# Kernel optimization log

Hardware: AMD Instinct MI355X
Metric: run time of the kernel (lower is better)

The kernel has to match this reference:

```python
import jax, jax.numpy as jnp
import numpy as np

NUM_HEADS = 12
HEAD_SIZE = 64
HIDDEN = NUM_HEADS * HEAD_SIZE  # 768
ONE_SIDED_WINDOW = 256          # attention_window 512 // 2
NEG = -10000.0


def setup_inputs() -> dict:
    key = jax.random.key(0)
    ks = jax.random.split(key, 16)
    B, W, E, H = 1, 2048, 128, HIDDEN
    std = 0.02
    def lin(kw, kb):
        return (jax.random.normal(kw, (H, H), jnp.float32) * std,
                jax.random.normal(kb, (H,), jnp.float32) * std)
    q_w, q_b = lin(ks[0], ks[1])
    k_w, k_b = lin(ks[2], ks[3])
    v_w, v_b = lin(ks[4], ks[5])
    w2e_w, w2e_b = lin(ks[6], ks[7])
    e2w_w, e2w_b = lin(ks[8], ks[9])
    e2e_w, e2e_b = lin(ks[10], ks[11])
    return {
        "word_hidden_states": jax.random.normal(ks[12], (B, W, H), jnp.float32),
        "entity_hidden_states": jax.random.normal(ks[13], (B, E, H), jnp.float32),
        "attention_mask": jnp.zeros((B, 1, 1, W + E), jnp.float32),
        "q_w": q_w, "q_b": q_b, "k_w": k_w, "k_b": k_b, "v_w": v_w, "v_b": v_b,
        "w2e_w": w2e_w, "w2e_b": w2e_b, "e2w_w": e2w_w, "e2w_b": e2w_b,
        "e2e_w": e2e_w, "e2e_b": e2e_b,
    }


def reference(word_hidden_states, entity_hidden_states, attention_mask,
              q_w, q_b, k_w, k_b, v_w, v_b,
              w2e_w, w2e_b, e2w_w, e2w_b, e2e_w, e2e_b):
    B, W, H = word_hidden_states.shape
    E = entity_hidden_states.shape[1]
    S = W + E

    def heads(x):  # [B, L, H] -> [B, nh, L, hd]
        return x.reshape(B, -1, NUM_HEADS, HEAD_SIZE).transpose(0, 2, 1, 3)

    concat = jnp.concatenate([word_hidden_states, entity_hidden_states], axis=1)
    k = heads(concat @ k_w + k_b)          # [B, nh, S, hd]
    v = heads(concat @ v_w + v_b)
    q_w2w = heads(word_hidden_states @ q_w + q_b)
    q_w2e = heads(word_hidden_states @ w2e_w + w2e_b)
    q_e2w = heads(entity_hidden_states @ e2w_w + e2w_b)
    q_e2e = heads(entity_hidden_states @ e2e_w + e2e_b)

    k_word, k_ent = k[:, :, :W], k[:, :, W:]

    # --- w2w: Longformer sliding-window QK^T, then _conversion to a dense
    # [B, nh, W, W] matrix with out-of-band entries set to -10000. ---
    w2w = jnp.einsum('bhid,bhjd->bhij', q_w2w, k_word)  # [B, nh, W, W]
    idx = jnp.arange(W)
    in_band = jnp.abs(idx[:, None] - idx[None, :]) <= ONE_SIDED_WINDOW  # [W, W]
    # diagonal mask: float_mask[j] (-10000 where attention_mask != 0) added
    # within the band (broadcast over heads / query positions)
    mask_words = attention_mask[:, 0, 0, :W]                # [B, W]
    float_mask = jnp.where(mask_words != 0.0, NEG, 0.0)     # [B, W]
    w2w = w2w + float_mask[:, None, None, :]
    # _conversion: out-of-band -> -10000; also exact zeros -> -10000 (source quirk)
    w2w = jnp.where(in_band[None, None] & (w2w != 0.0), w2w, NEG)

    # --- entity-aware dense blocks ---
    w2e = jnp.einsum('bhid,bhjd->bhij', q_w2e, k_ent)    # [B, nh, W, E]
    e2w = jnp.einsum('bhid,bhjd->bhij', q_e2w, k_word)   # [B, nh, E, W]
    e2e = jnp.einsum('bhid,bhjd->bhij', q_e2e, k_ent)    # [B, nh, E, E]

    word_scores = jnp.concatenate([w2w, w2e], axis=3)    # [B, nh, W, S]
    ent_scores = jnp.concatenate([e2w, e2e], axis=3)     # [B, nh, E, S]
    scores = jnp.concatenate([word_scores, ent_scores], axis=2)  # [B, nh, S, S]

    scores = scores / jnp.sqrt(jnp.float32(HEAD_SIZE)) + attention_mask
    probs = jax.nn.softmax(scores, axis=-1)

    ctx = jnp.einsum('bhij,bhjd->bhid', probs, v)        # [B, nh, S, hd]
    ctx = ctx.transpose(0, 2, 1, 3).reshape(B, S, H)
    return ctx[:, :W, :], ctx[:, W:, :]
```

## Files before the change

kernel.cpp:

```cpp
#include <hip/hip_runtime.h>

typedef __bf16 bf16x8 __attribute__((ext_vector_type(8)));
typedef unsigned short u16x8 __attribute__((ext_vector_type(8)));
typedef u16x8 u16x8_a __attribute__((may_alias));
typedef unsigned int u32x2 __attribute__((ext_vector_type(2)));
typedef u32x2 u32x2_a __attribute__((may_alias));
typedef unsigned int u32x4 __attribute__((ext_vector_type(4)));
typedef u32x4 u32x4_a __attribute__((may_alias));
typedef float f32x4 __attribute__((ext_vector_type(4)));

#define LOG2E 1.4426950408889634f
#define NEGV  -10000.0f

__device__ __forceinline__ unsigned short f2bf(float f){
  union{float f; unsigned int i;} x; x.f=f;
  unsigned int i = x.i;
  return (unsigned short)((i + 0x7FFFu + ((i>>16)&1u)) >> 16);
}
__device__ __forceinline__ u16x8 cvt8(float4 a, float4 b){
  u16x8 r;
  r[0]=f2bf(a.x); r[1]=f2bf(a.y); r[2]=f2bf(a.z); r[3]=f2bf(a.w);
  r[4]=f2bf(b.x); r[5]=f2bf(b.y); r[6]=f2bf(b.z); r[7]=f2bf(b.w);
  return r;
}
__device__ __forceinline__ bf16x8 ldb(const unsigned short* p){
  return __builtin_bit_cast(bf16x8, *(const u16x8_a*)p);
}

__global__ __launch_bounds__(256) void cast_a(
    const float* __restrict__ word, const float* __restrict__ ent,
    unsigned short* __restrict__ Abf)
{
  size_t e = ((size_t)blockIdx.x*256 + threadIdx.x)*8;
  const size_t WE = (size_t)2048*768;
  const float* s = (e < WE) ? (word + e) : (ent + (e - WE));
  float4 a = *(const float4*)s;
  float4 b = *(const float4*)(s+4);
  *(u16x8_a*)(Abf + e) = cvt8(a,b);
}

__global__ __launch_bounds__(256) void transpose6(
    const float* __restrict__ w0, const float* __restrict__ w1,
    const float* __restrict__ w2, const float* __restrict__ w3,
    const float* __restrict__ w4, const float* __restrict__ w5,
    unsigned short* __restrict__ outT)
{
  const float* src;
  switch (blockIdx.z){
    case 0: src = w0; break; case 1: src = w1; break; case 2: src = w2; break;
    case 3: src = w3; break; case 4: src = w4; break; default: src = w5; break;
  }
  unsigned short* dst = outT + (size_t)blockIdx.z * 589824;
  __shared__ float tile[32][33];
  int tx = threadIdx.x, ty = threadIdx.y;
  int x0 = blockIdx.x*32, y0 = blockIdx.y*32;
  #pragma unroll
  for (int i=0;i<32;i+=8) tile[ty+i][tx] = src[(size_t)(y0+ty+i)*768 + x0+tx];
  __syncthreads();
  #pragma unroll
  for (int i=0;i<32;i+=8) dst[(size_t)(x0+ty+i)*768 + y0+tx] = f2bf(tile[tx][ty+i]);
}

__global__ __launch_bounds__(256) void transpose_v(
    const unsigned short* __restrict__ Vb, unsigned short* __restrict__ VbT)
{
  __shared__ unsigned short t[32][33];
  int tx = threadIdx.x, ty = threadIdx.y;
  int x0 = blockIdx.x*32;
  int y0 = blockIdx.y*32;
  #pragma unroll
  for (int i=0;i<32;i+=8) t[ty+i][tx] = Vb[(size_t)(x0+ty+i)*768 + y0+tx];
  __syncthreads();
  #pragma unroll
  for (int i=0;i<32;i+=8) VbT[(size_t)(y0+ty+i)*2176 + x0+tx] = t[tx][ty+i];
}

__global__ __launch_bounds__(256) void gemm_proj(
    const unsigned short* __restrict__ Abf,
    const unsigned short* __restrict__ wT,
    const float* __restrict__ bK, const float* __restrict__ bV,
    const float* __restrict__ bQ, const float* __restrict__ bWE,
    const float* __restrict__ bEW, const float* __restrict__ bEE,
    unsigned short* __restrict__ oK, unsigned short* __restrict__ oV,
    unsigned short* __restrict__ oQ, unsigned short* __restrict__ oWE,
    unsigned short* __restrict__ oEW, unsigned short* __restrict__ oEE)
{
  int mt = blockIdx.x, ntile = blockIdx.y;
  int g, mg;
  if      (mt <  34){ g=0; mg=mt;     }
  else if (mt <  68){ g=1; mg=mt-34;  }
  else if (mt < 100){ g=2; mg=mt-68;  }
  else if (mt < 132){ g=3; mg=mt-100; }
  else if (mt < 134){ g=4; mg=mt-132; }
  else              { g=5; mg=mt-134; }
  int m0 = mg*64;
  const unsigned short* A = Abf + (size_t)((g>=4 ? 2048 : 0) + m0)*768;
  const unsigned short* B = wT + (size_t)g*589824;
  const float* bias; unsigned short* out;
  switch (g){
    case 0: bias=bK;  out=oK;  break;
    case 1: bias=bV;  out=oV;  break;
    case 2: bias=bQ;  out=oQ;  break;
    case 3: bias=bWE; out=oWE; break;
    case 4: bias=bEW; out=oEW; break;
    default:bias=bEE; out=oEE; break;
  }
  out += (size_t)m0*768;
  int n0 = ntile*128;

  __shared__ __align__(16) unsigned short a_s[64*32];
  __shared__ __align__(16) unsigned short b_s[128*32];

  int tid  = threadIdx.x;
  int w    = tid>>6, lane = tid&63, quad = lane>>4, lr = lane&15;
  int wm   = (w&1)*32, wn = (w>>1)*64;

  f32x4 acc[2][4];
  #pragma unroll
  for (int i=0;i<2;i++) for (int j=0;j<4;j++) for (int r=0;r<4;r++) acc[i][j][r]=0.f;

  int ar  = tid>>1;
  int ak2 = (tid&1)*16;
  int aar = tid>>2;
  int aak = (tid&3)*8;
  const unsigned short* Arow = A + (size_t)aar*768 + aak;
  const unsigned short* Brow = B + (size_t)(n0+ar)*768 + ak2;

  for (int k0=0; k0<768; k0+=32){
    u16x8 av  = *(const u16x8_a*)(Arow + k0);
    u16x8 bv0 = *(const u16x8_a*)(Brow + k0);
    u16x8 bv1 = *(const u16x8_a*)(Brow + k0 + 8);
    __syncthreads();
    *(u16x8_a*)(a_s + aar*32 + aak)    = av;
    *(u16x8_a*)(b_s + ar*32 + ak2)     = bv0;
    *(u16x8_a*)(b_s + ar*32 + ak2 + 8) = bv1;
    __syncthreads();
    bf16x8 af[2], bfr[4];
    #pragma unroll
    for (int i=0;i<2;i++) af[i]  = ldb(a_s + (wm+i*16+lr)*32 + quad*8);
    #pragma unroll
    for (int j=0;j<4;j++) bfr[j] = ldb(b_s + (wn+j*16+lr)*32 + quad*8);
    #pragma unroll
    for (int i=0;i<2;i++)
      #pragma unroll
      for (int j=0;j<4;j++)
        acc[i][j] = __builtin_amdgcn_mfma_f32_16x16x32_bf16(af[i], bfr[j], acc[i][j], 0,0,0);
  }
  #pragma unroll
  for (int j=0;j<4;j++){
    int col = n0 + wn + j*16 + lr;
    float bb = bias[col];
    #pragma unroll
    for (int i=0;i<2;i++){
      int rowb = wm + i*16 + quad*4;
      #pragma unroll
      for (int r=0;r<4;r++)
        out[(size_t)(rowb+r)*768 + col] = f2bf(acc[i][j][r] + bb);
    }
  }
}

__global__ __launch_bounds__(256) void attn_split(
  const unsigned short* __restrict__ Kb,  const unsigned short* __restrict__ VbT,
  const unsigned short* __restrict__ Qw,  const unsigned short* __restrict__ Qwe,
  const unsigned short* __restrict__ Qew, const unsigned short* __restrict__ Qee,
  const float* __restrict__ am,
  float* __restrict__ outw, float* __restrict__ pO, float* __restrict__ pML)
{
  int lin = blockIdx.x + 80*blockIdx.y;
  int wid = (lin & 7)*120 + (lin >> 3);
  int bx = wid % 80;
  int h  = wid / 80;

  int tid = threadIdx.x, w = tid>>6, lane = tid&63, quad = lane>>4, lr = lane&15;
  bool isword = bx < 64;
  int qrb, kh, nsplit, eg=0, ehalf=0;
  const unsigned short *Qa, *Qb;
  if (isword){ qrb = bx*32 + (w>>1)*16; kh = w&1; nsplit = 2; Qa=Qw;  Qb=Qwe; }
  else       { int e = bx-64; eg = e>>1; ehalf = e&1;
               qrb = eg*16;             kh = w;   nsplit = 4; Qa=Qew; Qb=Qee; }
  int hofs = h*64;

  __shared__ __align__(16) unsigned int shb[4*64*20];
  unsigned int* p32w = shb + w*320;

  const unsigned short* qr = Qa + (size_t)(qrb+lr)*768 + hofs + quad*8;
  bf16x8 qa0 = ldb(qr), qa1 = ldb(qr + 32);
  qr = Qb + (size_t)(qrb+lr)*768 + hofs + quad*8;
  bf16x8 qb0 = ldb(qr), qb1 = ldb(qr + 32);

  u16x8 onesu;
  #pragma unroll
  for (int i=0;i<8;i++) onesu[i] = 0x3F80;
  bf16x8 onesf = __builtin_bit_cast(bf16x8, onesu);

  float m = -1e30f;
  f32x4 o[4], l4;
  #pragma unroll
  for (int r=0;r<4;r++) l4[r] = 0.f;
  #pragma unroll
  for (int n2=0;n2<4;n2++) for (int r=0;r<4;r++) o[n2][r] = 0.f;

  int lo, nw, start, end, step;
  if (isword){
    lo = qrb - 256; if (lo < 0) lo = 0; lo &= ~31;
    int hi = qrb + 272; if (hi > 2048) hi = 2048; hi = (hi + 31) & ~31;
    nw = (hi - lo) >> 5;
    start = kh; end = nw + 4; step = 2;
  } else {
    lo = 0; nw = 64;
    start = ehalf*34 + kh; end = ehalf*34 + 34; step = 4;
  }
  int iq = qrb + lr;

  for (int c = start; c < end; c += step){
    bool entp = c >= nw;
    int j0 = entp ? (2048 + (c-nw)*32) : (lo + c*32);

    const unsigned short* kp = Kb + (size_t)(j0+lr)*768 + hofs + quad*8;
    bf16x8 k00 = ldb(kp),          k01 = ldb(kp + 32);
    bf16x8 k10 = ldb(kp + 16*768), k11 = ldb(kp + 16*768 + 32);
    const unsigned short* vp = VbT + (size_t)(hofs + lr)*2176 + j0 + quad*8;
    bf16x8 va0 = ldb(vp), va1 = ldb(vp + 16*2176), va2 = ldb(vp + 32*2176), va3 = ldb(vp + 48*2176);
    float4 am0 = *(const float4*)(am + j0 + quad*4);
    float4 am1 = *(const float4*)(am + j0 + 16 + quad*4);

    bf16x8 qf0 = entp ? qb0 : qa0;
    bf16x8 qf1 = entp ? qb1 : qa1;
    f32x4 st0 = {0.f,0.f,0.f,0.f}, st1 = {0.f,0.f,0.f,0.f};
    __builtin_amdgcn_s_setprio(1);
    st0 = __builtin_amdgcn_mfma_f32_16x16x32_bf16(k00, qf0, st0, 0,0,0);
    st0 = __builtin_amdgcn_mfma_f32_16x16x32_bf16(k01, qf1, st0, 0,0,0);
    st1 = __builtin_amdgcn_mfma_f32_16x16x32_bf16(k10, qf0, st1, 0,0,0);
    st1 = __builtin_amdgcn_mfma_f32_16x16x32_bf16(k11, qf1, st1, 0,0,0);
    __builtin_amdgcn_s_setprio(0);

    float sc0[4], sc1[4];
    bool wband = isword && !entp;
    #pragma unroll
    for (int r=0;r<4;r++){
      {
        float amj = am0[r];
        float sv  = st0[r];
        if (wband){
          sv += (amj != 0.f) ? NEGV : 0.f;
          int j = j0 + quad*4 + r;
          bool ok = ((unsigned)(iq - j + 256) <= 512u) && (sv != 0.f);
          sv = ok ? sv : NEGV;
        }
        sc0[r] = sv * (LOG2E*0.125f) + amj * LOG2E;
      }
      {
        float amj = am1[r];
        float sv  = st1[r];
        if (wband){
          sv += (amj != 0.f) ? NEGV : 0.f;
          int j = j0 + 16 + quad*4 + r;
          bool ok = ((unsigned)(iq - j + 256) <= 512u) && (sv != 0.f);
          sv = ok ? sv : NEGV;
        }
        sc1[r] = sv * (LOG2E*0.125f) + amj * LOG2E;
      }
    }

    float mx = fmaxf(fmaxf(fmaxf(sc0[0],sc0[1]), fmaxf(sc0[2],sc0[3])),
                     fmaxf(fmaxf(sc1[0],sc1[1]), fmaxf(sc1[2],sc1[3])));
    mx = fmaxf(mx, __shfl_xor(mx, 16));
    mx = fmaxf(mx, __shfl_xor(mx, 32));
    float mn = fmaxf(m, mx);
    float alpha = exp2f(m - mn);
    m = mn;

    float p00 = exp2f(sc0[0]-mn), p01 = exp2f(sc0[1]-mn);
    float p02 = exp2f(sc0[2]-mn), p03 = exp2f(sc0[3]-mn);
    float p10 = exp2f(sc1[0]-mn), p11 = exp2f(sc1[1]-mn);
    float p12 = exp2f(sc1[2]-mn), p13 = exp2f(sc1[3]-mn);
    unsigned int x0 = (unsigned int)f2bf(p00) | ((unsigned int)f2bf(p01)<<16);
    unsigned int x1 = (unsigned int)f2bf(p02) | ((unsigned int)f2bf(p03)<<16);
    unsigned int x2 = (unsigned int)f2bf(p10) | ((unsigned int)f2bf(p11)<<16);
    unsigned int x3 = (unsigned int)f2bf(p12) | ((unsigned int)f2bf(p13)<<16);

    #pragma unroll
    for (int r=0;r<4;r++) l4[r] *= alpha;
    #pragma unroll
    for (int n2=0;n2<4;n2++)
      #pragma unroll
      for (int r=0;r<4;r++) o[n2][r] *= alpha;

    unsigned int* row = p32w + lr*20;
    u32x2 w0v = {x0, x1};
    u32x2 w1v = {x2, x3};
    *(u32x2_a*)(row + quad*2)     = w0v;
    *(u32x2_a*)(row + 8 + quad*2) = w1v;
    bf16x8 pf = ldb((const unsigned short*)(p32w + lr*20 + quad*4));

    __builtin_amdgcn_s_setprio(1);
    o[0] = __builtin_amdgcn_mfma_f32_16x16x32_bf16(va0, pf, o[0], 0,0,0);
    o[1] = __builtin_amdgcn_mfma_f32_16x16x32_bf16(va1, pf, o[1], 0,0,0);
    o[2] = __builtin_amdgcn_mfma_f32_16x16x32_bf16(va2, pf, o[2], 0,0,0);
    o[3] = __builtin_amdgcn_mfma_f32_16x16x32_bf16(va3, pf, o[3], 0,0,0);
    l4   = __builtin_amdgcn_mfma_f32_16x16x32_bf16(onesf, pf, l4, 0,0,0);
    __builtin_amdgcn_s_setprio(0);
  }

  float lsc = l4[0];
  __syncthreads();
  {
    float* my = (float*)shb + ((size_t)(w*64 + lane))*20;
    my[0] = m; my[1] = lsc;
    #pragma unroll
    for (int n2=0;n2<4;n2++)
      #pragma unroll
      for (int r=0;r<4;r++) my[2+n2*4+r] = o[n2][r];
  }
  __syncthreads();
  if (kh == 0){
    for (int p=1; p<nsplit; p++){
      const float* pr = (float*)shb + ((size_t)((w+p)*64 + lane))*20;
      float m2 = pr[0], l2 = pr[1];
      float M  = fmaxf(m, m2);
      float e1 = exp2f(m-M), e2 = exp2f(m2-M);
      m = M;
      lsc = lsc*e1 + l2*e2;
      #pragma unroll
      for (int n2=0;n2<4;n2++)
        #pragma unroll
        for (int r=0;r<4;r++)
          o[n2][r] = o[n2][r]*e1 + pr[2+n2*4+r]*e2;
    }
    if (isword){
      float rinv = 1.f / lsc;
      #pragma unroll
      for (int n2=0;n2<4;n2++){
        float4 sv;
        sv.x = o[n2][0]*rinv; sv.y = o[n2][1]*rinv;
        sv.z = o[n2][2]*rinv; sv.w = o[n2][3]*rinv;
        *(float4*)(outw + (size_t)(qrb+lr)*768 + hofs + n2*16 + quad*4) = sv;
      }
    } else {
      int idx = (eg*12 + h)*2 + ehalf;
      float* po = pO + (size_t)idx*1024;
      #pragma unroll
      for (int n2=0;n2<4;n2++){
        float4 sv;
        sv.x = o[n2][0]; sv.y = o[n2][1]; sv.z = o[n2][2]; sv.w = o[n2][3];
        *(float4*)(po + lr*64 + n2*16 + quad*4) = sv;
      }
      if (quad == 0){
        float* pml = pML + (size_t)idx*32;
        pml[lr*2]     = m;
        pml[lr*2 + 1] = lsc;
      }
    }
  }
}

__global__ __launch_bounds__(256) void merge_ent(
    const float* __restrict__ pO, const float* __restrict__ pML,
    float* __restrict__ oute)
{
  int b = blockIdx.x;
  int g = b/12, h = b%12;
  int tid = threadIdx.x;
  int row = tid>>4, cg = tid&15;
  int i0 = b*2, i1 = b*2+1;
  float m0 = pML[(size_t)i0*32 + row*2], l0 = pML[(size_t)i0*32 + row*2 + 1];
  float m1 = pML[(size_t)i1*32 + row*2], l1 = pML[(size_t)i1*32 + row*2 + 1];
  float M  = fmaxf(m0, m1);
  float e0 = exp2f(m0-M), e1 = exp2f(m1-M);
  float rl = 1.f/(l0*e0 + l1*e1);
  float4 a = *(const float4*)(pO + (size_t)i0*1024 + row*64 + cg*4);
  float4 c = *(const float4*)(pO + (size_t)i1*1024 + row*64 + cg*4);
  float4 o;
  o.x = (a.x*e0 + c.x*e1)*rl;
  o.y = (a.y*e0 + c.y*e1)*rl;
  o.z = (a.z*e0 + c.z*e1)*rl;
  o.w = (a.w*e0 + c.w*e1)*rl;
  *(float4*)(oute + (size_t)(g*16+row)*768 + h*64 + cg*4) = o;
}

extern "C" void kernel_launch(void* const* d_in, const int* in_sizes, int n_in,
                              void* d_out, int out_size, void* d_ws, size_t ws_size,
                              hipStream_t stream) {
  const float* word  = (const float*)d_in[0];
  const float* ent   = (const float*)d_in[1];
  const float* am    = (const float*)d_in[2];
  const float* q_w   = (const float*)d_in[3];
  const float* q_b   = (const float*)d_in[4];
  const float* k_w   = (const float*)d_in[5];
  const float* k_b   = (const float*)d_in[6];
  const float* v_w   = (const float*)d_in[7];
  const float* v_b   = (const float*)d_in[8];
  const float* w2e_w = (const float*)d_in[9];
  const float* w2e_b = (const float*)d_in[10];
  const float* e2w_w = (const float*)d_in[11];
  const float* e2w_b = (const float*)d_in[12];
  const float* e2e_w = (const float*)d_in[13];
  const float* e2e_b = (const float*)d_in[14];

  unsigned short* ws  = (unsigned short*)d_ws;
  unsigned short* wT  = ws;
  unsigned short* Kb  = wT  + (size_t)6*589824;
  unsigned short* Vb  = Kb  + (size_t)2176*768;
  unsigned short* Qw  = Vb  + (size_t)2176*768;
  unsigned short* Qwe = Qw  + (size_t)2048*768;
  unsigned short* Qew = Qwe + (size_t)2048*768;
  unsigned short* Qee = Qew + (size_t)128*768;
  unsigned short* VbT = Qee + (size_t)128*768;
  unsigned short* Abf = VbT + (size_t)768*2176;

  float* pO  = (float*)wT;
  float* pML = pO + (size_t)192*1024;

  float* outw = (float*)d_out;
  float* oute = outw + (size_t)2048*768;

  hipLaunchKernelGGL(cast_a, dim3(816), dim3(256), 0, stream, word, ent, Abf);
  hipLaunchKernelGGL(transpose6, dim3(24,24,6), dim3(32,8), 0, stream,
                     k_w, v_w, q_w, w2e_w, e2w_w, e2e_w, wT);
  hipLaunchKernelGGL(gemm_proj, dim3(136,6), dim3(256), 0, stream,
                     Abf, wT, k_b, v_b, q_b, w2e_b, e2w_b, e2e_b,
                     Kb, Vb, Qw, Qwe, Qew, Qee);
  hipLaunchKernelGGL(transpose_v, dim3(68,24), dim3(32,8), 0, stream, Vb, VbT);
  hipLaunchKernelGGL(attn_split, dim3(80,12), dim3(256), 0, stream,
                     Kb, VbT, Qw, Qwe, Qew, Qee, am, outw, pO, pML);
  hipLaunchKernelGGL(merge_ent, dim3(96), dim3(256), 0, stream,
                     pO, pML, oute);
}
```

Before: 180.6 us.

## Process two key chunks per attention iteration and use direct global-to-LDS loads in GEMM

The attention loop now handles two 32-key chunks per iteration. It issues both sets of K loads up front, computes one shared running max and rescale, and does two PV MFMA passes, with the second V load issued between them. This halves the per-chunk softmax rescale and reduction overhead and adds memory-level parallelism, at the cost of more registers and a masked tail when the chunk count is odd. The projection GEMM replaces its register-staged global-to-LDS copies with global_load_lds direct transfers, and the LDS stride for the partial-result merge is padded to 21.

```diff
diff --git a/kernel.cpp b/kernel.cpp
--- a/kernel.cpp
+++ b/kernel.cpp
@@ -25,6 +25,11 @@
 }
 __device__ __forceinline__ bf16x8 ldb(const unsigned short* p){
   return __builtin_bit_cast(bf16x8, *(const u16x8_a*)p);
+}
+__device__ __forceinline__ void gload16(const unsigned short* g, unsigned short* l){
+  __builtin_amdgcn_global_load_lds(
+    (const __attribute__((address_space(1))) void*)g,
+    (__attribute__((address_space(3))) void*)l, 16, 0, 0);
 }
 
 __global__ __launch_bounds__(256) void cast_a(
@@ -119,21 +124,20 @@
   #pragma unroll
   for (int i=0;i<2;i++) for (int j=0;j<4;j++) for (int r=0;r<4;r++) acc[i][j][r]=0.f;
 
-  int ar  = tid>>1;
-  int ak2 = (tid&1)*16;
-  int aar = tid>>2;
-  int aak = (tid&3)*8;
-  const unsigned short* Arow = A + (size_t)aar*768 + aak;
-  const unsigned short* Brow = B + (size_t)(n0+ar)*768 + ak2;
+  int srow = lane>>2;
+  int scol = (lane&3)*8;
+  const unsigned short* gA  = A + (size_t)(w*16 + srow)*768 + scol;
+  const unsigned short* gB0 = B + (size_t)(n0 + w*32 + srow)*768 + scol;
+  const unsigned short* gB1 = gB0 + (size_t)16*768;
+  unsigned short* lA  = a_s + w*16*32;
+  unsigned short* lB0 = b_s + w*32*32;
+  unsigned short* lB1 = b_s + w*32*32 + 16*32;
 
   for (int k0=0; k0<768; k0+=32){
-    u16x8 av  = *(const u16x8_a*)(Arow + k0);
-    u16x8 bv0 = *(const u16x8_a*)(Brow + k0);
-    u16x8 bv1 = *(const u16x8_a*)(Brow + k0 + 8);
     __syncthreads();
-    *(u16x8_a*)(a_s + aar*32 + aak)    = av;
-    *(u16x8_a*)(b_s + ar*32 + ak2)     = bv0;
-    *(u16x8_a*)(b_s + ar*32 + ak2 + 8) = bv1;
+    gload16(gA  + k0, lA);
+    gload16(gB0 + k0, lB0);
+    gload16(gB1 + k0, lB1);
     __syncthreads();
     bf16x8 af[2], bfr[4];
     #pragma unroll
@@ -181,8 +185,8 @@
                qrb = eg*16;             kh = w;   nsplit = 4; Qa=Qew; Qb=Qee; }
   int hofs = h*64;
 
-  __shared__ __align__(16) unsigned int shb[4*64*20];
-  unsigned int* p32w = shb + w*320;
+  __shared__ __align__(16) unsigned int shb[4*64*21];
+  unsigned int* p32w = shb + w*(16*44);
 
   const unsigned short* qr = Qa + (size_t)(qrb+lr)*768 + hofs + quad*8;
   bf16x8 qa0 = ldb(qr), qa1 = ldb(qr + 32);
@@ -213,72 +217,97 @@
   }
   int iq = qrb + lr;
 
-  for (int c = start; c < end; c += step){
-    bool entp = c >= nw;
-    int j0 = entp ? (2048 + (c-nw)*32) : (lo + c*32);
-
-    const unsigned short* kp = Kb + (size_t)(j0+lr)*768 + hofs + quad*8;
-    bf16x8 k00 = ldb(kp),          k01 = ldb(kp + 32);
-    bf16x8 k10 = ldb(kp + 16*768), k11 = ldb(kp + 16*768 + 32);
-    const unsigned short* vp = VbT + (size_t)(hofs + lr)*2176 + j0 + quad*8;
-    bf16x8 va0 = ldb(vp), va1 = ldb(vp + 16*2176), va2 = ldb(vp + 32*2176), va3 = ldb(vp + 48*2176);
-    float4 am0 = *(const float4*)(am + j0 + quad*4);
-    float4 am1 = *(const float4*)(am + j0 + 16 + quad*4);
-
-    bf16x8 qf0 = entp ? qb0 : qa0;
-    bf16x8 qf1 = entp ? qb1 : qa1;
-    f32x4 st0 = {0.f,0.f,0.f,0.f}, st1 = {0.f,0.f,0.f,0.f};
+  for (int c = start; c < end; c += 2*step){
+    int c2r = c + step;
+    bool ph = (c2r >= end);
+    int c2 = ph ? c : c2r;
+
+    bool entp1 = c  >= nw;  int j1 = entp1 ? (2048 + (c -nw)*32) : (lo + c *32);
+    bool entp2 = c2 >= nw;  int j2 = entp2 ? (2048 + (c2-nw)*32) : (lo + c2*32);
+
+    const unsigned short* kp1 = Kb + (size_t)(j1+lr)*768 + hofs + quad*8;
+    bf16x8 kA0 = ldb(kp1),          kA1 = ldb(kp1 + 32);
+    bf16x8 kA2 = ldb(kp1 + 16*768), kA3 = ldb(kp1 + 16*768 + 32);
+    const unsigned short* kp2 = Kb + (size_t)(j2+lr)*768 + hofs + quad*8;
+    bf16x8 kB0 = ldb(kp2),          kB1 = ldb(kp2 + 32);
+    bf16x8 kB2 = ldb(kp2 + 16*768), kB3 = ldb(kp2 + 16*768 + 32);
+    const unsigned short* vp1 = VbT + (size_t)(hofs + lr)*2176 + j1 + quad*8;
+    bf16x8 v10 = ldb(vp1), v11 = ldb(vp1 + 16*2176), v12 = ldb(vp1 + 32*2176), v13 = ldb(vp1 + 48*2176);
+    float4 amA0 = *(const float4*)(am + j1 + quad*4);
+    float4 amA1 = *(const float4*)(am + j1 + 16 + quad*4);
+    float4 amB0 = *(const float4*)(am + j2 + quad*4);
+    float4 amB1 = *(const float4*)(am + j2 + 16 + quad*4);
+
+    bf16x8 qf10 = entp1 ? qb0 : qa0, qf11 = entp1 ? qb1 : qa1;
+    bf16x8 qf20 = entp2 ? qb0 : qa0, qf21 = entp2 ? qb1 : qa1;
+
+    f32x4 sA0 = {0.f,0.f,0.f,0.f}, sA1 = {0.f,0.f,0.f,0.f};
+    f32x4 sB0 = {0.f,0.f,0.f,0.f}, sB1 = {0.f,0.f,0.f,0.f};
     __builtin_amdgcn_s_setprio(1);
-    st0 = __builtin_amdgcn_mfma_f32_16x16x32_bf16(k00, qf0, st0, 0,0,0);
-    st0 = __builtin_amdgcn_mfma_f32_16x16x32_bf16(k01, qf1, st0, 0,0,0);
-    st1 = __builtin_amdgcn_mfma_f32_16x16x32_bf16(k10, qf0, st1, 0,0,0);
-    st1 = __builtin_amdgcn_mfma_f32_16x16x32_bf16(k11, qf1, st1, 0,0,0);
+    sA0 = __builtin_amdgcn_mfma_f32_16x16x32_bf16(kA0, qf10, sA0, 0,0,0);
+    sA0 = __builtin_amdgcn_mfma_f32_16x16x32_bf16(kA1, qf11, sA0, 0,0,0);
+    sA1 = __builtin_amdgcn_mfma_f32_16x16x32_bf16(kA2, qf10, sA1, 0,0,0);
+    sA1 = __builtin_amdgcn_mfma_f32_16x16x32_bf16(kA3, qf11, sA1, 0,0,0);
+    sB0 = __builtin_amdgcn_mfma_f32_16x16x32_bf16(kB0, qf20, sB0, 0,0,0);
+    sB0 = __builtin_amdgcn_mfma_f32_16x16x32_bf16(kB1, qf21, sB0, 0,0,0);
+    sB1 = __builtin_amdgcn_mfma_f32_16x16x32_bf16(kB2, qf20, sB1, 0,0,0);
+    sB1 = __builtin_amdgcn_mfma_f32_16x16x32_bf16(kB3, qf21, sB1, 0,0,0);
     __builtin_amdgcn_s_setprio(0);
 
-    float sc0[4], sc1[4];
-    bool wband = isword && !entp;
+    float scA0[4], scA1[4], scB0[4], scB1[4];
+    bool wb1 = isword && !entp1;
+    bool wb2 = isword && !entp2;
     #pragma unroll
     for (int r=0;r<4;r++){
-      {
-        float amj = am0[r];
-        float sv  = st0[r];
-        if (wband){
-          sv += (amj != 0.f) ? NEGV : 0.f;
-          int j = j0 + quad*4 + r;
+      { float amj = amA0[r], sv = sA0[r];
+        if (wb1){ sv += (amj != 0.f) ? NEGV : 0.f;
+          int j = j1 + quad*4 + r;
           bool ok = ((unsigned)(iq - j + 256) <= 512u) && (sv != 0.f);
-          sv = ok ? sv : NEGV;
-        }
-        sc0[r] = sv * (LOG2E*0.125f) + amj * LOG2E;
-      }
-      {
-        float amj = am1[r];
-        float sv  = st1[r];
-        if (wband){
-          sv += (amj != 0.f) ? NEGV : 0.f;
-          int j = j0 + 16 + quad*4 + r;
+          sv = ok ? sv : NEGV; }
+        scA0[r] = sv * (LOG2E*0.125f) + amj * LOG2E; }
+      { float amj = amA1[r], sv = sA1[r];
+        if (wb1){ sv += (amj != 0.f) ? NEGV : 0.f;
+          int j = j1 + 16 + quad*4 + r;
           bool ok = ((unsigned)(iq - j + 256) <= 512u) && (sv != 0.f);
-          sv = ok ? sv : NEGV;
-        }
-        sc1[r] = sv * (LOG2E*0.125f) + amj * LOG2E;
-      }
+          sv = ok ? sv : NEGV; }
+        scA1[r] = sv * (LOG2E*0.125f) + amj * LOG2E; }
+      { float amj = amB0[r], sv = sB0[r];
+        if (wb2){ sv += (amj != 0.f) ? NEGV : 0.f;
+          int j = j2 + quad*4 + r;
+          bool ok = ((unsigned)(iq - j + 256) <= 512u) && (sv != 0.f);
+          sv = ok ? sv : NEGV; }
+        scB0[r] = sv * (LOG2E*0.125f) + amj * LOG2E; }
+      { float amj = amB1[r], sv = sB1[r];
+        if (wb2){ sv += (amj != 0.f) ? NEGV : 0.f;
+          int j = j2 + 16 + quad*4 + r;
+          bool ok = ((unsigned)(iq - j + 256) <= 512u) && (sv != 0.f);
+          sv = ok ? sv : NEGV; }
+        scB1[r] = sv * (LOG2E*0.125f) + amj * LOG2E; }
     }
-
-    float mx = fmaxf(fmaxf(fmaxf(sc0[0],sc0[1]), fmaxf(sc0[2],sc0[3])),
-                     fmaxf(fmaxf(sc1[0],sc1[1]), fmaxf(sc1[2],sc1[3])));
+    if (ph){
+      #pragma unroll
+      for (int r=0;r<4;r++){ scB0[r] = -1e30f; scB1[r] = -1e30f; }
+    }
+
+    float mx = fmaxf(
+      fmaxf(fmaxf(fmaxf(scA0[0],scA0[1]), fmaxf(scA0[2],scA0[3])),
+            fmaxf(fmaxf(scA1[0],scA1[1]), fmaxf(scA1[2],scA1[3]))),
+      fmaxf(fmaxf(fmaxf(scB0[0],scB0[1]), fmaxf(scB0[2],scB0[3])),
+            fmaxf(fmaxf(scB1[0],scB1[1]), fmaxf(scB1[2],scB1[3]))));
     mx = fmaxf(mx, __shfl_xor(mx, 16));
     mx = fmaxf(mx, __shfl_xor(mx, 32));
     float mn = fmaxf(m, mx);
     float alpha = exp2f(m - mn);
     m = mn;
 
-    float p00 = exp2f(sc0[0]-mn), p01 = exp2f(sc0[1]-mn);
-    float p02 = exp2f(sc0[2]-mn), p03 = exp2f(sc0[3]-mn);
-    float p10 = exp2f(sc1[0]-mn), p11 = exp2f(sc1[1]-mn);
-    float p12 = exp2f(sc1[2]-mn), p13 = exp2f(sc1[3]-mn);
-    unsigned int x0 = (unsigned int)f2bf(p00) | ((unsigned int)f2bf(p01)<<16);
-    unsigned int x1 = (unsigned int)f2bf(p02) | ((unsigned int)f2bf(p03)<<16);
-    unsigned int x2 = (unsigned int)f2bf(p10) | ((unsigned int)f2bf(p11)<<16);
-    unsigned int x3 = (unsigned int)f2bf(p12) | ((unsigned int)f2bf(p13)<<16);
+    unsigned int xA0 = (unsigned int)f2bf(exp2f(scA0[0]-mn)) | ((unsigned int)f2bf(exp2f(scA0[1]-mn))<<16);
+    unsigned int xA1 = (unsigned int)f2bf(exp2f(scA0[2]-mn)) | ((unsigned int)f2bf(exp2f(scA0[3]-mn))<<16);
+    unsigned int xA2 = (unsigned int)f2bf(exp2f(scA1[0]-mn)) | ((unsigned int)f2bf(exp2f(scA1[1]-mn))<<16);
+    unsigned int xA3 = (unsigned int)f2bf(exp2f(scA1[2]-mn)) | ((unsigned int)f2bf(exp2f(scA1[3]-mn))<<16);
+    unsigned int xB0 = (unsigned int)f2bf(exp2f(scB0[0]-mn)) | ((unsigned int)f2bf(exp2f(scB0[1]-mn))<<16);
+    unsigned int xB1 = (unsigned int)f2bf(exp2f(scB0[2]-mn)) | ((unsigned int)f2bf(exp2f(scB0[3]-mn))<<16);
+    unsigned int xB2 = (unsigned int)f2bf(exp2f(scB1[0]-mn)) | ((unsigned int)f2bf(exp2f(scB1[1]-mn))<<16);
+    unsigned int xB3 = (unsigned int)f2bf(exp2f(scB1[2]-mn)) | ((unsigned int)f2bf(exp2f(scB1[3]-mn))<<16);
 
     #pragma unroll
     for (int r=0;r<4;r++) l4[r] *= alpha;
@@ -287,26 +316,42 @@
       #pragma unroll
       for (int r=0;r<4;r++) o[n2][r] *= alpha;
 
-    unsigned int* row = p32w + lr*20;
-    u32x2 w0v = {x0, x1};
-    u32x2 w1v = {x2, x3};
-    *(u32x2_a*)(row + quad*2)     = w0v;
-    *(u32x2_a*)(row + 8 + quad*2) = w1v;
-    bf16x8 pf = ldb((const unsigned short*)(p32w + lr*20 + quad*4));
+    unsigned int* row = p32w + lr*44;
+    u32x2 wv0 = {xA0, xA1};
+    u32x2 wv1 = {xA2, xA3};
+    u32x2 wv2 = {xB0, xB1};
+    u32x2 wv3 = {xB2, xB3};
+    *(u32x2_a*)(row + quad*2)      = wv0;
+    *(u32x2_a*)(row + 8  + quad*2) = wv1;
+    *(u32x2_a*)(row + 16 + quad*2) = wv2;
+    *(u32x2_a*)(row + 24 + quad*2) = wv3;
+    bf16x8 pf1 = ldb((const unsigned short*)(p32w + lr*44 + quad*4));
+    bf16x8 pf2 = ldb((const unsigned short*)(p32w + lr*44 + 16 + quad*4));
 
     __builtin_amdgcn_s_setprio(1);
-    o[0] = __builtin_amdgcn_mfma_f32_16x16x32_bf16(va0, pf, o[0], 0,0,0);
-    o[1] = __builtin_amdgcn_mfma_f32_16x16x32_bf16(va1, pf, o[1], 0,0,0);
-    o[2] = __builtin_amdgcn_mfma_f32_16x16x32_bf16(va2, pf, o[2], 0,0,0);
-    o[3] = __builtin_amdgcn_mfma_f32_16x16x32_bf16(va3, pf, o[3], 0,0,0);
-    l4   = __builtin_amdgcn_mfma_f32_16x16x32_bf16(onesf, pf, l4, 0,0,0);
+    o[0] = __builtin_amdgcn_mfma_f32_16x16x32_bf16(v10, pf1, o[0], 0,0,0);
+    o[1] = __builtin_amdgcn_mfma_f32_16x16x32_bf16(v11, pf1, o[1], 0,0,0);
+    o[2] = __builtin_amdgcn_mfma_f32_16x16x32_bf16(v12, pf1, o[2], 0,0,0);
+    o[3] = __builtin_amdgcn_mfma_f32_16x16x32_bf16(v13, pf1, o[3], 0,0,0);
+    l4   = __builtin_amdgcn_mfma_f32_16x16x32_bf16(onesf, pf1, l4, 0,0,0);
+    __builtin_amdgcn_s_setprio(0);
+
+    const unsigned short* vp2 = VbT + (size_t)(hofs + lr)*2176 + j2 + quad*8;
+    bf16x8 v20 = ldb(vp2), v21 = ldb(vp2 + 16*2176), v22 = ldb(vp2 + 32*2176), v23 = ldb(vp2 + 48*2176);
+
+    __builtin_amdgcn_s_setprio(1);
+    o[0] = __builtin_amdgcn_mfma_f32_16x16x32_bf16(v20, pf2, o[0], 0,0,0);
+    o[1] = __builtin_amdgcn_mfma_f32_16x16x32_bf16(v21, pf2, o[1], 0,0,0);
+    o[2] = __builtin_amdgcn_mfma_f32_16x16x32_bf16(v22, pf2, o[2], 0,0,0);
+    o[3] = __builtin_amdgcn_mfma_f32_16x16x32_bf16(v23, pf2, o[3], 0,0,0);
+    l4   = __builtin_amdgcn_mfma_f32_16x16x32_bf16(onesf, pf2, l4, 0,0,0);
     __builtin_amdgcn_s_setprio(0);
   }
 
   float lsc = l4[0];
   __syncthreads();
   {
-    float* my = (float*)shb + ((size_t)(w*64 + lane))*20;
+    float* my = (float*)shb + ((size_t)(w*64 + lane))*21;
     my[0] = m; my[1] = lsc;
     #pragma unroll
     for (int n2=0;n2<4;n2++)
@@ -316,7 +361,7 @@
   __syncthreads();
   if (kh == 0){
     for (int p=1; p<nsplit; p++){
-      const float* pr = (float*)shb + ((size_t)((w+p)*64 + lane))*20;
+      const float* pr = (float*)shb + ((size_t)((w+p)*64 + lane))*21;
       float m2 = pr[0], l2 = pr[1];
       float M  = fmaxf(m, m2);
       float e1 = exp2f(m-M), e2 = exp2f(m2-M);
```

Result: faster. 172.8 us (-4.3%).
